# Kernel tuning notes

Measured on AMD Instinct MI355X. Metric: run time of the kernel, lower is better.

The kernel has to match this reference:

```python
import jax, jax.numpy as jnp
import numpy as np

D = 512; H = 8; L = 4; V = 32000; MAXSEQ = 512; B = 8; T = 511; FF = 256; HEAD_H = 32; HD = D // H
NEG = -1e9  # finite stand-in for -inf key-padding mask (entmax output is exactly 0 there)


def setup_inputs():
    key = jax.random.key(0)
    ks = jax.random.split(key, 16)
    def n(k, shape, s=0.02):
        return jax.random.normal(k, shape, jnp.float32) * s
    return {
        "x": jax.random.randint(ks[0], (B, T), 0, V + 1),
        "embed_tab": n(ks[1], (V + 1, D)).at[0].set(0.0),  # padding_idx=0 row zeroed
        "pos_tab": n(ks[2], (MAXSEQ, D)),
        "cls": jax.random.normal(ks[3], (1, 1, D), jnp.float32),
        "Wq": n(ks[4], (L, D, D)),  # stored (in,out): y = x @ W
        "Wk": n(ks[5], (L, D, D)),
        "Wv": n(ks[6], (L, D, D)),
        "Wo": n(ks[7], (L, D, D)),
        "an_g": jnp.ones((L, D)), "an_b": jnp.zeros((L, D)),
        "ln1_g": jnp.ones((L, D)), "ln1_b": jnp.zeros((L, D)),
        "ln2_g": jnp.ones((L, D)), "ln2_b": jnp.zeros((L, D)),
        "f1_w": n(ks[8], (L, D, FF)), "f1_b": jnp.zeros((L, FF)),
        "f2_w": n(ks[9], (L, FF, D)), "f2_b": jnp.zeros((L, D)),
        "h1_w": n(ks[10], (D, HEAD_H)), "h1_b": jnp.zeros((HEAD_H,)),
        "h2_w": n(ks[11], (HEAD_H, 1)), "h2_b": jnp.zeros((1,)),
    }


def _ln(x, g, b, eps=1e-5):
    m = jnp.mean(x, -1, keepdims=True)
    v = jnp.mean((x - m) ** 2, -1, keepdims=True)
    return (x - m) * jax.lax.rsqrt(v + eps) * g + b


def entmax15(x):
    # Exact alpha=1.5 entmax along last axis (Peters et al., 2019), fully vectorized.
    x = x / 2.0
    x = x - jnp.max(x, -1, keepdims=True)  # shift-invariance for stability
    xs = -jnp.sort(-x, axis=-1)            # descending sort
    d = x.shape[-1]
    rho = jnp.arange(1, d + 1, dtype=x.dtype)
    mean = jnp.cumsum(xs, -1) / rho
    meansq = jnp.cumsum(xs * xs, -1) / rho
    ss = rho * (meansq - mean * mean)
    delta = jnp.maximum((1.0 - ss) / rho, 0.0)
    tau = mean - jnp.sqrt(delta)
    support = jnp.sum((tau <= xs).astype(jnp.int32), axis=-1, keepdims=True)
    tau_star = jnp.take_along_axis(tau, support - 1, axis=-1)
    return jnp.maximum(x - tau_star, 0.0) ** 2


def _forward(x, embed_tab, pos_tab, cls, Wq, Wk, Wv, Wo, an_g, an_b, ln1_g, ln1_b, ln2_g, ln2_b, f1_w, f1_b, f2_w, f2_b, h1_w, h1_b, h2_w, h2_b):
    Bx, Tx = x.shape
    # padding_idx: zero embedding AND zero grad for pad tokens via mask multiply
    h = embed_tab[x] * (x != 0)[..., None].astype(embed_tab.dtype) + pos_tab[:Tx]
    h = jnp.concatenate([jnp.broadcast_to(cls, (Bx, 1, D)), h], axis=1)  # [B, Tc, D]
    pad = jnp.concatenate([jnp.zeros((Bx, 1), bool), x == 0], axis=1)     # [B, Tc]
    Tc = Tx + 1
    scale = jnp.asarray(np.sqrt(HD), jnp.float32)
    for l in range(L):
        xin = _ln(h, ln1_g[l], ln1_b[l])
        def split(y):
            return y.reshape(Bx, Tc, H, HD).transpose(0, 2, 1, 3)  # [B,H,Tc,hd]
        q = split(xin @ Wq[l]); k = split(xin @ Wk[l]); v = split(xin @ Wv[l])
        scores = jnp.einsum('bhqd,bhkd->bhqk', q, k) / scale
        scores = jnp.where(pad[:, None, None, :], NEG, scores)
        A = entmax15(scores)
        o = jnp.einsum('bhqk,bhkd->bhqd', A, v).transpose(0, 2, 1, 3).reshape(Bx, Tc, D)
        h = _ln(o @ Wo[l] + xin, an_g[l], an_b[l]) + h        # attn residual (post-LN inside layer + outer residual)
        y = _ln(h, ln2_g[l], ln2_b[l])
        y = jax.nn.gelu(y @ f1_w[l] + f1_b[l], approximate=False) @ f2_w[l] + f2_b[l]
        h = y + h
    z = jax.nn.relu(h[:, 0] @ h1_w + h1_b)
    return (z @ h2_w + h2_b)[:, 0]  # [B]


def reference(x, embed_tab, pos_tab, cls, Wq, Wk, Wv, Wo, an_g, an_b, ln1_g, ln1_b, ln2_g, ln2_b, f1_w, f1_b, f2_w, f2_b, h1_w, h1_b, h2_w, h2_b):
    return _forward(x, embed_tab, pos_tab, cls, Wq, Wk, Wv, Wo, an_g, an_b, ln1_g, ln1_b, ln2_g, ln2_b, f1_w, f1_b, f2_w, f2_b, h1_w, h1_b, h2_w, h2_b)
```

## Files before the change

### kernel.cpp

```cpp
#include <hip/hip_runtime.h>
#include <hip/hip_bf16.h>
#include <math.h>

#define BB    8
#define TT    511
#define TC    512
#define DD    512
#define HH    8
#define HD    64
#define LL    4
#define FF    256
#define HEADH 32
#define NTOK  (BB*TC)

typedef __bf16 bf16x8 __attribute__((ext_vector_type(8)));
typedef float  f32x4  __attribute__((ext_vector_type(4)));

__device__ __forceinline__ unsigned short f2b(float v) {
  __bf16 t = (__bf16)v;
  return __builtin_bit_cast(unsigned short, t);
}
__device__ __forceinline__ float gelu_f(float x) {
  return 0.5f * x * (1.0f + erff(x * 0.7071067811865476f));
}

template<int CTRL>
__device__ __forceinline__ float dppmov(float x) {
  return __builtin_bit_cast(float,
      __builtin_amdgcn_update_dpp(0, __builtin_bit_cast(int, x), CTRL, 0xF, 0xF, true));
}
__device__ __forceinline__ float wsum(float v) {
  v += dppmov<0xB1>(v);
  v += dppmov<0x4E>(v);
  v += dppmov<0x141>(v);
  v += dppmov<0x140>(v);
  v += __builtin_bit_cast(float, __builtin_amdgcn_ds_swizzle(__builtin_bit_cast(int, v), 0x401F));
  float a = __builtin_bit_cast(float, __builtin_amdgcn_readlane(__builtin_bit_cast(int, v), 0));
  float b = __builtin_bit_cast(float, __builtin_amdgcn_readlane(__builtin_bit_cast(int, v), 32));
  return a + b;
}

__device__ __forceinline__ void stage_rows(char* lds, const char* g, size_t gstride,
                                           int nIss, int wid, int nw, int lane) {
  for (int is = wid; is < nIss; is += nw) {
    const int row = (is << 3) + (lane >> 3);
    const int s = lane & 7;
    const char* gp = g + (size_t)row * gstride + (((s ^ (row & 7))) << 4);
    __builtin_amdgcn_global_load_lds((const __attribute__((address_space(1))) void*)gp,
                                     (__attribute__((address_space(3))) void*)(lds + ((size_t)is << 10)),
                                     16, 0, 0);
  }
}
__device__ __forceinline__ bf16x8 frag_ld(const char* lds, int row, int kslot) {
  return *(const bf16x8*)(lds + row * 128 + ((kslot ^ (row & 7)) << 4));
}

__global__ void embed_k(const int* __restrict__ x, const float* __restrict__ etab,
                        const float* __restrict__ ptab, const float* __restrict__ cls,
                        float* __restrict__ h, float* __restrict__ padf) {
  const int tok = blockIdx.x;
  const int b = tok >> 9, t = tok & 511;
  const int lane = threadIdx.x;
  float4 o0, o1;
  int isPad = 0;
  if (t == 0) {
    o0 = ((const float4*)cls)[lane];
    o1 = ((const float4*)cls)[64 + lane];
  } else {
    const int id = x[b * TT + (t - 1)];
    isPad = (id == 0);
    const float m = isPad ? 0.0f : 1.0f;
    const float4* e  = (const float4*)(etab + (size_t)id * DD);
    const float4* pp = (const float4*)(ptab + (size_t)(t - 1) * DD);
    float4 e0 = e[lane], e1 = e[64 + lane];
    float4 p0 = pp[lane], p1 = pp[64 + lane];
    o0.x = e0.x * m + p0.x; o0.y = e0.y * m + p0.y;
    o0.z = e0.z * m + p0.z; o0.w = e0.w * m + p0.w;
    o1.x = e1.x * m + p1.x; o1.y = e1.y * m + p1.y;
    o1.z = e1.z * m + p1.z; o1.w = e1.w * m + p1.w;
  }
  float4* hp = (float4*)(h + (size_t)tok * DD);
  hp[lane] = o0; hp[64 + lane] = o1;
  if (lane == 0) padf[tok] = isPad ? -5.0e8f : 0.0f;
}

__global__ __launch_bounds__(256) void wprep(const float* __restrict__ Wq, const float* __restrict__ Wk,
                                             const float* __restrict__ Wv, const float* __restrict__ Wo,
                                             const float* __restrict__ f1w, const float* __restrict__ f2w,
                                             unsigned short* __restrict__ qkvT, unsigned short* __restrict__ woT,
                                             unsigned short* __restrict__ f1T, unsigned short* __restrict__ f2T) {
  const int z = blockIdx.z;
  const float* src; unsigned short* dst; int K, N;
  if (z < 12) { int l = z / 3, w = z % 3;
    src = (w == 0 ? Wq : w == 1 ? Wk : Wv) + (size_t)l * 512 * 512; K = 512; N = 512;
    dst = qkvT + (size_t)l * 1536 * 512 + (size_t)w * 512 * 512;
  } else if (z < 16) { int l = z - 12; src = Wo + (size_t)l * 512 * 512; K = 512; N = 512;
    dst = woT + (size_t)l * 512 * 512;
  } else if (z < 20) { int l = z - 16; src = f1w + (size_t)l * 512 * 256; K = 512; N = 256;
    dst = f1T + (size_t)l * 256 * 512;
  } else { int l = z - 20; src = f2w + (size_t)l * 256 * 512; K = 256; N = 512;
    dst = f2T + (size_t)l * 512 * 256;
  }
  const int n0 = blockIdx.x * 32, k0 = blockIdx.y * 32;
  if (n0 >= N || k0 >= K) return;
  __shared__ float tbuf[32][33];
  const int tx = threadIdx.x & 31, ty = threadIdx.x >> 5;
#pragma unroll
  for (int i = 0; i < 32; i += 8)
    tbuf[ty + i][tx] = src[(size_t)(k0 + ty + i) * N + n0 + tx];
  __syncthreads();
#pragma unroll
  for (int i = 0; i < 32; i += 8)
    dst[(size_t)(n0 + ty + i) * K + k0 + tx] = f2b(tbuf[tx][ty + i]);
}

__global__ __launch_bounds__(256) void ln_rows(const float* __restrict__ in,
                                               float* __restrict__ outf,
                                               unsigned short* __restrict__ outb,
                                               const float* __restrict__ g,
                                               const float* __restrict__ b) {
  const int wave = threadIdx.x >> 6, lane = threadIdx.x & 63;
  const int row = blockIdx.x * 4 + wave;
  const float* p = in + (size_t)row * DD;
  float4 a = ((const float4*)p)[lane];
  float4 c = ((const float4*)p)[64 + lane];
  float v[8] = {a.x, a.y, a.z, a.w, c.x, c.y, c.z, c.w};
  float s = 0.f;
#pragma unroll
  for (int i = 0; i < 8; ++i) s += v[i];
  const float m = wsum(s) * (1.0f / 512.0f);
  float sq = 0.f;
#pragma unroll
  for (int i = 0; i < 8; ++i) { float d = v[i] - m; sq = fmaf(d, d, sq); }
  const float rs = rsqrtf(wsum(sq) * (1.0f / 512.0f) + 1e-5f);
  float4 g0 = ((const float4*)g)[lane], g1 = ((const float4*)g)[64 + lane];
  float4 b0 = ((const float4*)b)[lane], b1 = ((const float4*)b)[64 + lane];
  float r[8];
  r[0] = (v[0] - m) * rs * g0.x + b0.x; r[1] = (v[1] - m) * rs * g0.y + b0.y;
  r[2] = (v[2] - m) * rs * g0.z + b0.z; r[3] = (v[3] - m) * rs * g0.w + b0.w;
  r[4] = (v[4] - m) * rs * g1.x + b1.x; r[5] = (v[5] - m) * rs * g1.y + b1.y;
  r[6] = (v[6] - m) * rs * g1.z + b1.z; r[7] = (v[7] - m) * rs * g1.w + b1.w;
  float4* op = (float4*)(outf + (size_t)row * DD);
  op[lane] = make_float4(r[0], r[1], r[2], r[3]);
  op[64 + lane] = make_float4(r[4], r[5], r[6], r[7]);
  ushort4 q0, q1;
  q0.x = f2b(r[0]); q0.y = f2b(r[1]); q0.z = f2b(r[2]); q0.w = f2b(r[3]);
  q1.x = f2b(r[4]); q1.y = f2b(r[5]); q1.z = f2b(r[6]); q1.w = f2b(r[7]);
  ushort4* ob = (ushort4*)(outb + (size_t)row * DD);
  ob[lane] = q0; ob[64 + lane] = q1;
}

__global__ __launch_bounds__(256) void resid_ln2(const float* __restrict__ t,
                                                 const float* __restrict__ xin,
                                                 float* __restrict__ h,
                                                 const float* __restrict__ g1,
                                                 const float* __restrict__ b1,
                                                 const float* __restrict__ g2,
                                                 const float* __restrict__ b2,
                                                 unsigned short* __restrict__ xinb) {
  const int wave = threadIdx.x >> 6, lane = threadIdx.x & 63;
  const int row = blockIdx.x * 4 + wave;
  const float* tp = t + (size_t)row * DD;
  const float* xp = xin + (size_t)row * DD;
  float4 t0 = ((const float4*)tp)[lane], t1 = ((const float4*)tp)[64 + lane];
  float4 x0 = ((const float4*)xp)[lane], x1 = ((const float4*)xp)[64 + lane];
  float v[8] = {t0.x + x0.x, t0.y + x0.y, t0.z + x0.z, t0.w + x0.w,
                t1.x + x1.x, t1.y + x1.y, t1.z + x1.z, t1.w + x1.w};
  float s = 0.f;
#pragma unroll
  for (int i = 0; i < 8; ++i) s += v[i];
  const float m = wsum(s) * (1.0f / 512.0f);
  float sq = 0.f;
#pragma unroll
  for (int i = 0; i < 8; ++i) { float d = v[i] - m; sq = fmaf(d, d, sq); }
  const float rs = rsqrtf(wsum(sq) * (1.0f / 512.0f) + 1e-5f);
  float4 g0 = ((const float4*)g1)[lane], g1v = ((const float4*)g1)[64 + lane];
  float4 c0 = ((const float4*)b1)[lane], c1 = ((const float4*)b1)[64 + lane];
  float4* hp = (float4*)(h + (size_t)row * DD);
  float4 h0 = hp[lane], h1 = hp[64 + lane];
  float a[8];
  a[0] = h0.x + (v[0] - m) * rs * g0.x + c0.x;  a[1] = h0.y + (v[1] - m) * rs * g0.y + c0.y;
  a[2] = h0.z + (v[2] - m) * rs * g0.z + c0.z;  a[3] = h0.w + (v[3] - m) * rs * g0.w + c0.w;
  a[4] = h1.x + (v[4] - m) * rs * g1v.x + c1.x; a[5] = h1.y + (v[5] - m) * rs * g1v.y + c1.y;
  a[6] = h1.z + (v[6] - m) * rs * g1v.z + c1.z; a[7] = h1.w + (v[7] - m) * rs * g1v.w + c1.w;
  hp[lane] = make_float4(a[0], a[1], a[2], a[3]);
  hp[64 + lane] = make_float4(a[4], a[5], a[6], a[7]);
  float s2 = 0.f;
#pragma unroll
  for (int i = 0; i < 8; ++i) s2 += a[i];
  const float m2 = wsum(s2) * (1.0f / 512.0f);
  float sq2 = 0.f;
#pragma unroll
  for (int i = 0; i < 8; ++i) { float d = a[i] - m2; sq2 = fmaf(d, d, sq2); }
  const float rs2 = rsqrtf(wsum(sq2) * (1.0f / 512.0f) + 1e-5f);
  float4 G0 = ((const float4*)g2)[lane], G1 = ((const float4*)g2)[64 + lane];
  float4 B0 = ((const float4*)b2)[lane], B1 = ((const float4*)b2)[64 + lane];
  ushort4 q0, q1;
  q0.x = f2b((a[0] - m2) * rs2 * G0.x + B0.x); q0.y = f2b((a[1] - m2) * rs2 * G0.y + B0.y);
  q0.z = f2b((a[2] - m2) * rs2 * G0.z + B0.z); q0.w = f2b((a[3] - m2) * rs2 * G0.w + B0.w);
  q1.x = f2b((a[4] - m2) * rs2 * G1.x + B1.x); q1.y = f2b((a[5] - m2) * rs2 * G1.y + B1.y);
  q1.z = f2b((a[6] - m2) * rs2 * G1.z + B1.z); q1.w = f2b((a[7] - m2) * rs2 * G1.w + B1.w);
  ushort4* ob = (ushort4*)(xinb + (size_t)row * DD);
  ob[lane] = q0; ob[64 + lane] = q1;
}

template<int BM, int BN, int WM, int WN, int EPI>
__global__ __launch_bounds__(256) void mgemm(const unsigned short* __restrict__ A,
                                             const unsigned short* __restrict__ Bt,
                                             void* __restrict__ C0, void* __restrict__ C1,
                                             void* __restrict__ C2,
                                             const float* __restrict__ bias,
                                             int M, int N, int K) {
  constexpr int NW = (BM / WM) * (BN / WN);
  constexpr int FM = WM / 16, FN = WN / 16;
  __shared__ char smem[(BM + BN) * 128];
  char* sA = smem; char* sB = smem + BM * 128;
  const int tid = threadIdx.x, lane = tid & 63, wid = tid >> 6;
  const int row0 = blockIdx.y * BM, col0 = blockIdx.x * BN;
  const int wrow = (wid / (BN / WN)) * WM, wcol = (wid % (BN / WN)) * WN;
  f32x4 acc[FM][FN] = {};
  const char* Ag = (const char*)(A + (size_t)row0 * K);
  const char* Bg = (const char*)(Bt + (size_t)col0 * K);
  for (int k0 = 0; k0 < K; k0 += 64) {
    __syncthreads();
    stage_rows(sA, Ag + (size_t)k0 * 2, (size_t)K * 2, BM / 8, wid, NW, lane);
    stage_rows(sB, Bg + (size_t)k0 * 2, (size_t)K * 2, BN / 8, wid, NW, lane);
    __syncthreads();
#pragma unroll
    for (int kk = 0; kk < 2; ++kk) {
      bf16x8 af[FM], bfr[FN];
#pragma unroll
      for (int mi = 0; mi < FM; ++mi)
        af[mi] = frag_ld(sA, wrow + mi * 16 + (lane & 15), kk * 4 + (lane >> 4));
#pragma unroll
      for (int ni = 0; ni < FN; ++ni)
        bfr[ni] = frag_ld(sB, wcol + ni * 16 + (lane & 15), kk * 4 + (lane >> 4));
#pragma unroll
      for (int mi = 0; mi < FM; ++mi)
#pragma unroll
        for (int ni = 0; ni < FN; ++ni)
          acc[mi][ni] = __builtin_amdgcn_mfma_f32_16x16x32_bf16(af[mi], bfr[ni], acc[mi][ni], 0, 0, 0);
    }
  }
#pragma unroll
  for (int mi = 0; mi < FM; ++mi)
#pragma unroll
    for (int ni = 0; ni < FN; ++ni) {
      const int colb = col0 + wcol + ni * 16;
      const int col = colb + (lane & 15);
      const int rowb = row0 + wrow + mi * 16 + (lane >> 4) * 4;
      if (EPI == 1 && (colb >> 9) == 2) {
        const int cc = col - 1024, hh = cc >> 6, d = cc & 63, b = rowb >> 9, t = rowb & 511;
        ushort4 pk;
        pk.x = f2b(acc[mi][ni][0]); pk.y = f2b(acc[mi][ni][1]);
        pk.z = f2b(acc[mi][ni][2]); pk.w = f2b(acc[mi][ni][3]);
        *(ushort4*)((unsigned short*)C2 + (((size_t)(b * 8 + hh) * 64 + d) << 9) + t) = pk;
      } else {
#pragma unroll
        for (int r = 0; r < 4; ++r) {
          const int row = rowb + r;
          const float v = acc[mi][ni][r];
          if (EPI == 0) {
            ((float*)C0)[(size_t)row * N + col] = v;
          } else if (EPI == 1) {
            if (colb < 512) ((unsigned short*)C0)[(size_t)row * 512 + col] = f2b(v);
            else            ((unsigned short*)C1)[(size_t)row * 512 + (col - 512)] = f2b(v);
          } else if (EPI == 2) {
            ((unsigned short*)C0)[(size_t)row * N + col] = f2b(gelu_f(v + bias[col]));
          } else {
            ((float*)C0)[(size_t)row * N + col] += v + bias[col];
          }
        }
      }
    }
}

__global__ __launch_bounds__(256, 2) void attn_fused(const unsigned short* __restrict__ q,
                                                     const unsigned short* __restrict__ k,
                                                     const unsigned short* __restrict__ vt,
                                                     const float* __restrict__ padf,
                                                     unsigned short* __restrict__ attnout) {
  __shared__ char sP[4][2048];
  const int bh = blockIdx.y, b = bh >> 3, hh = bh & 7;
  const int wid = threadIdx.x >> 6, lane = threadIdx.x & 63;
  const int q0 = blockIdx.x * 64 + wid * 16;
  const int col16 = lane & 15, g4 = lane >> 4;
  const unsigned short* qb = q + ((size_t)(b * TC + q0)) * DD + hh * HD;
  const unsigned short* kb = k + ((size_t)(b * TC)) * DD + hh * HD;
  const unsigned short* vb = vt + ((size_t)bh * 64) * 512;

  f32x4 acc[32] = {};
  const unsigned short* qrow = qb + (size_t)col16 * DD + g4 * 8;
  bf16x8 aq0 = *(const bf16x8*)(qrow);
  bf16x8 aq1 = *(const bf16x8*)(qrow + 32);
#pragma unroll
  for (int ni = 0; ni < 32; ++ni) {
    const unsigned short* krow = kb + (size_t)(16 * ni + col16) * DD + g4 * 8;
    bf16x8 b0 = *(const bf16x8*)(krow);
    bf16x8 b1 = *(const bf16x8*)(krow + 32);
    acc[ni] = __builtin_amdgcn_mfma_f32_16x16x32_bf16(aq0, b0, acc[ni], 0, 0, 0);
    acc[ni] = __builtin_amdgcn_mfma_f32_16x16x32_bf16(aq1, b1, acc[ni], 0, 0, 0);
  }

  const int btc = b * TC;
  float mx[4] = {-3.4e38f, -3.4e38f, -3.4e38f, -3.4e38f};
#pragma unroll
  for (int ni = 0; ni < 32; ++ni) {
    const float ma = padf[btc + 16 * ni + col16];
#pragma unroll
    for (int r = 0; r < 4; ++r) {
      acc[ni][r] = fmaf(acc[ni][r], 0.0625f, ma);
      mx[r] = fmaxf(mx[r], acc[ni][r]);
    }
  }
#pragma unroll
  for (int r = 0; r < 4; ++r) {
#pragma unroll
    for (int m = 1; m <= 8; m <<= 1) mx[r] = fmaxf(mx[r], __shfl_xor(mx[r], m, 64));
  }
#pragma unroll
  for (int ni = 0; ni < 32; ++ni)
#pragma unroll
    for (int r = 0; r < 4; ++r) acc[ni][r] -= mx[r];

  float tau[4] = {-1.f, -1.f, -1.f, -1.f};
  for (int it = 0; it < 8; ++it) {
    float s1[4] = {0, 0, 0, 0}, s2[4] = {0, 0, 0, 0};
#pragma unroll
    for (int ni = 0; ni < 32; ++ni)
#pragma unroll
      for (int r = 0; r < 4; ++r) {
        const float d = fmaxf(acc[ni][r] - tau[r], 0.f);
        s1[r] += d; s2[r] = fmaf(d, d, s2[r]);
      }
#pragma unroll
    for (int r = 0; r < 4; ++r) {
#pragma unroll
      for (int m = 1; m <= 8; m <<= 1) {
        s1[r] += __shfl_xor(s1[r], m, 64);
        s2[r] += __shfl_xor(s2[r], m, 64);
      }
      tau[r] += (s2[r] - 1.0f) / (2.0f * fmaxf(s1[r], 1e-20f));
    }
  }
  {
    float c1[4] = {0, 0, 0, 0}, s1[4] = {0, 0, 0, 0}, s2[4] = {0, 0, 0, 0};
#pragma unroll
    for (int ni = 0; ni < 32; ++ni)
#pragma unroll
      for (int r = 0; r < 4; ++r) {
        const float vv = acc[ni][r];
        const float msk = (vv > tau[r]) ? 1.0f : 0.0f;
        c1[r] += msk; s1[r] += msk * vv; s2[r] = fmaf(msk * vv, vv, s2[r]);
      }
#pragma unroll
    for (int r = 0; r < 4; ++r) {
#pragma unroll
      for (int m = 1; m <= 8; m <<= 1) {
        c1[r] += __shfl_xor(c1[r], m, 64);
        s1[r] += __shfl_xor(s1[r], m, 64);
        s2[r] += __shfl_xor(s2[r], m, 64);
      }
      const float disc = fmaxf(s1[r] * s1[r] - c1[r] * s2[r] + c1[r], 0.f);
      tau[r] = (s1[r] - sqrtf(disc)) / c1[r];
    }
  }
  float inv[4];
  {
    float ss[4] = {0, 0, 0, 0};
#pragma unroll
    for (int ni = 0; ni < 32; ++ni)
#pragma unroll
      for (int r = 0; r < 4; ++r) {
        const float d = fmaxf(acc[ni][r] - tau[r], 0.f);
        acc[ni][r] = d * d;
        ss[r] = fmaf(d, d, ss[r]);
      }
#pragma unroll
    for (int r = 0; r < 4; ++r) {
#pragma unroll
      for (int m = 1; m <= 8; m <<= 1) ss[r] += __shfl_xor(ss[r], m, 64);
      inv[r] = 1.0f / ss[r];
    }
  }

  char* myP = sP[wid];
  f32x4 acc2[4] = {};
#pragma unroll
  for (int c = 0; c < 8; ++c) {
#pragma unroll
    for (int nj = 0; nj < 4; ++nj) {
      const int ni = 4 * c + nj;
#pragma unroll
      for (int r = 0; r < 4; ++r) {
        const int lq = g4 * 4 + r;
        const int ck = nj * 16 + col16;
        *(unsigned short*)(myP + lq * 128 + ((((ck >> 3) ^ (lq & 7))) << 4) + ((ck & 7) << 1)) =
            f2b(acc[ni][r] * inv[r]);
      }
    }
#pragma unroll
    for (int kk = 0; kk < 2; ++kk) {
      const bf16x8 pa = frag_ld(myP, col16, kk * 4 + g4);
#pragma unroll
      for (int n2 = 0; n2 < 4; ++n2) {
        const unsigned short* vrow = vb + (size_t)(16 * n2 + col16) * 512 + c * 64 + kk * 32 + g4 * 8;
        acc2[n2] = __builtin_amdgcn_mfma_f32_16x16x32_bf16(pa, *(const bf16x8*)vrow, acc2[n2], 0, 0, 0);
      }
    }
  }
#pragma unroll
  for (int n2 = 0; n2 < 4; ++n2)
#pragma unroll
    for (int r = 0; r < 4; ++r)
      attnout[((size_t)(b * TC + q0 + g4 * 4 + r)) * DD + hh * HD + 16 * n2 + col16] = f2b(acc2[n2][r]);
}

__global__ void head_k(const float* __restrict__ h, const float* __restrict__ w1,
                       const float* __restrict__ b1, const float* __restrict__ w2,
                       const float* __restrict__ b2, float* __restrict__ out) {
  __shared__ float z[BB][HEADH];
  const int tid = threadIdx.x;
  const int b = tid >> 5, j = tid & 31;
  const float* hr = h + (size_t)(b * TC) * DD;
  float s = 0.f;
  for (int kk = 0; kk < DD; ++kk) s = fmaf(hr[kk], w1[kk * HEADH + j], s);
  z[b][j] = fmaxf(s + b1[j], 0.f);
  __syncthreads();
  if (tid < BB) {
    float acc = b2[0];
#pragma unroll
    for (int q2 = 0; q2 < HEADH; ++q2) acc = fmaf(z[tid][q2], w2[q2], acc);
    out[tid] = acc;
  }
}

#define WS_NEED 58736640ull
static __device__ __align__(256) unsigned char g_fallback_ws[WS_NEED];

extern "C" void kernel_launch(void* const* d_in, const int* in_sizes, int n_in,
                              void* d_out, int out_size, void* d_ws, size_t ws_size,
                              hipStream_t stream) {
  const int*   x     = (const int*)d_in[0];
  const float* etab  = (const float*)d_in[1];
  const float* ptab  = (const float*)d_in[2];
  const float* cls   = (const float*)d_in[3];
  const float* Wq    = (const float*)d_in[4];
  const float* Wk    = (const float*)d_in[5];
  const float* Wv    = (const float*)d_in[6];
  const float* Wo    = (const float*)d_in[7];
  const float* an_g  = (const float*)d_in[8];
  const float* an_b  = (const float*)d_in[9];
  const float* ln1_g = (const float*)d_in[10];
  const float* ln1_b = (const float*)d_in[11];
  const float* ln2_g = (const float*)d_in[12];
  const float* ln2_b = (const float*)d_in[13];
  const float* f1_w  = (const float*)d_in[14];
  const float* f1_b  = (const float*)d_in[15];
  const float* f2_w  = (const float*)d_in[16];
  const float* f2_b  = (const float*)d_in[17];
  const float* h1_w  = (const float*)d_in[18];
  const float* h1_b  = (const float*)d_in[19];
  const float* h2_w  = (const float*)d_in[20];
  const float* h2_b  = (const float*)d_in[21];
  float* out = (float*)d_out;

  void* wsbase = d_ws;
  if (ws_size < WS_NEED) hipGetSymbolAddress(&wsbase, HIP_SYMBOL(g_fallback_ws));
  char* base = (char*)wsbase;
  const size_t MB = 1048576;
  float* h_    = (float*)(base);
  float* xin_  = (float*)(base + 8 * MB);
  float* t_    = (float*)(base + 16 * MB);
  unsigned short* xinb_ = (unsigned short*)(base + 24 * MB);
  unsigned short* q_    = (unsigned short*)(base + 28 * MB);
  unsigned short* k_    = (unsigned short*)(base + 32 * MB);
  unsigned short* vt_   = (unsigned short*)(base + 36 * MB);
  unsigned short* at_   = (unsigned short*)(base + 40 * MB);
  unsigned short* mid_  = (unsigned short*)(base + 44 * MB);
  unsigned short* qkvT_ = (unsigned short*)(base + 46 * MB);
  unsigned short* woT_  = (unsigned short*)(base + 52 * MB);
  unsigned short* f1T_  = (unsigned short*)(base + 54 * MB);
  unsigned short* f2T_  = (unsigned short*)(base + 55 * MB);
  float* padf_ = (float*)(base + 56 * MB);

  wprep<<<dim3(16, 16, 24), 256, 0, stream>>>(Wq, Wk, Wv, Wo, f1_w, f2_w, qkvT_, woT_, f1T_, f2T_);
  embed_k<<<NTOK, 64, 0, stream>>>(x, etab, ptab, cls, h_, padf_);

  for (int l = 0; l < LL; ++l) {
    ln_rows<<<NTOK / 4, 256, 0, stream>>>(h_, xin_, xinb_, ln1_g + l * DD, ln1_b + l * DD);
    mgemm<128, 128, 64, 64, 1><<<dim3(12, 32), 256, 0, stream>>>(
        xinb_, qkvT_ + (size_t)l * 1536 * 512, q_, k_, vt_, nullptr, NTOK, 1536, 512);
    attn_fused<<<dim3(TC / 64, BB * HH), 256, 0, stream>>>(q_, k_, vt_, padf_, at_);
    mgemm<128, 128, 64, 64, 0><<<dim3(4, 32), 256, 0, stream>>>(
        at_, woT_ + (size_t)l * 512 * 512, t_, nullptr, nullptr, nullptr, NTOK, 512, 512);
    resid_ln2<<<NTOK / 4, 256, 0, stream>>>(t_, xin_, h_, an_g + l * DD, an_b + l * DD,
                                            ln2_g + l * DD, ln2_b + l * DD, xinb_);
    mgemm<64, 64, 32, 32, 2><<<dim3(4, 64), 256, 0, stream>>>(
        xinb_, f1T_ + (size_t)l * 256 * 512, mid_, nullptr, nullptr, f1_b + l * FF, NTOK, 256, 512);
    mgemm<64, 128, 32, 64, 3><<<dim3(4, 64), 256, 0, stream>>>(
        mid_, f2T_ + (size_t)l * 512 * 256, h_, nullptr, nullptr, f2_b + l * DD, NTOK, 512, 256);
  }

  head_k<<<1, 256, 0, stream>>>(h_, h1_w, h1_b, h2_w, h2_b, out);
}
```

Measured before the change: 607.0 us.

## Stage per-head K and V tiles in LDS and trim entmax iterations

The attention kernel now loads the whole per-head K block into a 64KB swizzled LDS buffer with global_load_lds and shares it across the four waves. After QK^T it reuses the same buffer for V, with a separate swizzle, instead of having every wave read K and V straight from global memory. The entmax threshold solve no longer subtracts the row max from every score. It starts tau at max-1 and runs 6 iterations instead of 8. This cuts redundant global/L2 traffic and ALU work, at the cost of extra block barriers, about 72KB of LDS per block that may limit occupancy, and some risk to threshold accuracy from fewer iterations.

New measurement: 545.1 us. 1.11x faster.

```diff
diff --git a/kernel.cpp b/kernel.cpp
--- a/kernel.cpp
+++ b/kernel.cpp
@@ -53,6 +53,20 @@
 }
 __device__ __forceinline__ bf16x8 frag_ld(const char* lds, int row, int kslot) {
   return *(const bf16x8*)(lds + row * 128 + ((kslot ^ (row & 7)) << 4));
+}
+__device__ __forceinline__ void stage_rows_v(char* lds, const char* g,
+                                             int nIss, int wid, int nw, int lane) {
+  for (int is = wid; is < nIss; is += nw) {
+    const int row = (is << 3) + (lane >> 3);
+    const int s = lane & 7;
+    const char* gp = g + (size_t)row * 128 + (((s ^ (is & 7))) << 4);
+    __builtin_amdgcn_global_load_lds((const __attribute__((address_space(1))) void*)gp,
+                                     (__attribute__((address_space(3))) void*)(lds + ((size_t)is << 10)),
+                                     16, 0, 0);
+  }
+}
+__device__ __forceinline__ bf16x8 frag_ld_v(const char* lds, int row, int kslot) {
+  return *(const bf16x8*)(lds + row * 128 + ((kslot ^ ((row >> 3) & 7)) << 4));
 }
 
 __global__ void embed_k(const int* __restrict__ x, const float* __restrict__ etab,
@@ -280,6 +294,7 @@
                                                      const unsigned short* __restrict__ vt,
                                                      const float* __restrict__ padf,
                                                      unsigned short* __restrict__ attnout) {
+  __shared__ char sKV[65536];
   __shared__ char sP[4][2048];
   const int bh = blockIdx.y, b = bh >> 3, hh = bh & 7;
   const int wid = threadIdx.x >> 6, lane = threadIdx.x & 63;
@@ -289,18 +304,24 @@
   const unsigned short* kb = k + ((size_t)(b * TC)) * DD + hh * HD;
   const unsigned short* vb = vt + ((size_t)bh * 64) * 512;
 
-  f32x4 acc[32] = {};
+  stage_rows(sKV, (const char*)kb, 1024, 64, wid, 4, lane);
   const unsigned short* qrow = qb + (size_t)col16 * DD + g4 * 8;
   bf16x8 aq0 = *(const bf16x8*)(qrow);
   bf16x8 aq1 = *(const bf16x8*)(qrow + 32);
+  __syncthreads();
+
+  f32x4 acc[32] = {};
 #pragma unroll
   for (int ni = 0; ni < 32; ++ni) {
-    const unsigned short* krow = kb + (size_t)(16 * ni + col16) * DD + g4 * 8;
-    bf16x8 b0 = *(const bf16x8*)(krow);
-    bf16x8 b1 = *(const bf16x8*)(krow + 32);
+    const int krow = 16 * ni + col16;
+    bf16x8 b0 = frag_ld(sKV, krow, g4);
+    bf16x8 b1 = frag_ld(sKV, krow, 4 + g4);
     acc[ni] = __builtin_amdgcn_mfma_f32_16x16x32_bf16(aq0, b0, acc[ni], 0, 0, 0);
     acc[ni] = __builtin_amdgcn_mfma_f32_16x16x32_bf16(aq1, b1, acc[ni], 0, 0, 0);
   }
+  __syncthreads();
+
+  stage_rows_v(sKV, (const char*)vb, 64, wid, 4, lane);
 
   const int btc = b * TC;
   float mx[4] = {-3.4e38f, -3.4e38f, -3.4e38f, -3.4e38f};
@@ -318,13 +339,9 @@
 #pragma unroll
     for (int m = 1; m <= 8; m <<= 1) mx[r] = fmaxf(mx[r], __shfl_xor(mx[r], m, 64));
   }
-#pragma unroll
-  for (int ni = 0; ni < 32; ++ni)
-#pragma unroll
-    for (int r = 0; r < 4; ++r) acc[ni][r] -= mx[r];
-
-  float tau[4] = {-1.f, -1.f, -1.f, -1.f};
-  for (int it = 0; it < 8; ++it) {
+
+  float tau[4] = {mx[0] - 1.f, mx[1] - 1.f, mx[2] - 1.f, mx[3] - 1.f};
+  for (int it = 0; it < 6; ++it) {
     float s1[4] = {0, 0, 0, 0}, s2[4] = {0, 0, 0, 0};
 #pragma unroll
     for (int ni = 0; ni < 32; ++ni)
@@ -383,6 +400,7 @@
       inv[r] = 1.0f / ss[r];
     }
   }
+  __syncthreads();
 
   char* myP = sP[wid];
   f32x4 acc2[4] = {};
@@ -404,8 +422,8 @@
       const bf16x8 pa = frag_ld(myP, col16, kk * 4 + g4);
 #pragma unroll
       for (int n2 = 0; n2 < 4; ++n2) {
-        const unsigned short* vrow = vb + (size_t)(16 * n2 + col16) * 512 + c * 64 + kk * 32 + g4 * 8;
-        acc2[n2] = __builtin_amdgcn_mfma_f32_16x16x32_bf16(pa, *(const bf16x8*)vrow, acc2[n2], 0, 0, 0);
+        const bf16x8 vv = frag_ld_v(sKV, (16 * n2 + col16) * 8 + c, kk * 4 + g4);
+        acc2[n2] = __builtin_amdgcn_mfma_f32_16x16x32_bf16(pa, vv, acc2[n2], 0, 0, 0);
       }
     }
   }
```
